# Kernel tuning notes

Measured on AMD Instinct MI355X. Metric: run time of the kernel, lower is better.

The kernel has to match this reference:

```python
import jax, jax.numpy as jnp
import numpy as np

B, E, XD = 2, 196608, 128     # batch, num edges (fine nodes), per-edge node feature dim
EIN, EOUT = 4, 128            # edge embedder dims
NREC = 12288                  # receiver (coarse) node count = 12*32^2
LIN, LOUT = EOUT + XD, 256    # output FFN dims


def setup_inputs() -> dict:
    key = jax.random.key(0)
    ks = jax.random.split(key, 8)
    w = lambda k, sh: jax.random.normal(k, sh, jnp.float32) * 0.05
    return {
        "x": jax.random.normal(ks[0], (B, E, XD), jnp.float32),
        "edge_attr": jax.random.normal(ks[1], (E, EIN), jnp.float32),
        "edge_index": jax.random.randint(ks[2], (2, E), 0, NREC, jnp.int32),
        # edge_embedder MLP: Linear(EIN,EOUT) -> SiLU -> Linear(EOUT,EOUT)
        "W1": w(ks[3], (EIN, EOUT)), "b1": jnp.zeros((EOUT,), jnp.float32),
        "W2": w(ks[4], (EOUT, EOUT)), "b2": jnp.zeros((EOUT,), jnp.float32),
        # output FeedForward: Linear(LIN,LOUT) -> SiLU -> Linear(LOUT,LOUT)
        "L1": w(ks[5], (LIN, LOUT)), "c1": jnp.zeros((LOUT,), jnp.float32),
        "L2": w(ks[6], (LOUT, LOUT)), "c2": jnp.zeros((LOUT,), jnp.float32),
    }


def reference(x, edge_attr, edge_index, W1, b1, W2, b2, L1, c1, L2, c2):
    # Edge MLP embed: [E, EIN] -> [E, EOUT]
    h = jax.nn.silu(edge_attr @ W1 + b1) @ W2 + b2
    # Broadcast edge features over batch and concat with per-edge node features
    ef = jnp.broadcast_to(h[None], (x.shape[0], h.shape[0], h.shape[1]))
    v = jnp.concatenate([ef, x], axis=-1)                 # [B, E, EOUT+XD]
    recv = edge_index[1]                                  # [E] in [0, NREC)
    # scatter_sum over edges -> receiver nodes, per batch
    agg = jax.vmap(lambda vb: jax.ops.segment_sum(vb, recv, num_segments=NREC))(v)  # [B, NREC, LIN]
    # Output FFN
    return jax.nn.silu(agg @ L1 + c1) @ L2 + c2           # [B, NREC, LOUT]
```

## Files before the change

### kernel.cpp

```cpp
#include <hip/hip_runtime.h>
#include <hip/hip_bf16.h>
#include <cstdint>
#include <cstddef>

#define B_     2
#define E_     196608
#define XD_    128
#define NREC_  12288
#define EOUT_  128
#define LIN_   256
#define LOUT_  256
#define M_     (B_ * NREC_)

typedef __attribute__((ext_vector_type(8))) short short8;
typedef __attribute__((ext_vector_type(4))) float f32x4;

__device__ __forceinline__ unsigned short f2bf(float f) {
    union { float f; unsigned u; } v; v.f = f;
    unsigned r = v.u + 0x7FFFu + ((v.u >> 16) & 1u);
    return (unsigned short)(r >> 16);
}

__global__ __launch_bounds__(256) void convert_w(const float* __restrict__ L1,
                                                 const float* __restrict__ L2,
                                                 unsigned short* __restrict__ L1T,
                                                 unsigned short* __restrict__ L2T) {
    int idx = blockIdx.x * 256 + threadIdx.x;
    int k = idx >> 8, n = idx & 255;
    L1T[n * 256 + k] = f2bf(L1[idx]);
    L2T[n * 256 + k] = f2bf(L2[idx]);
}

__global__ __launch_bounds__(256) void count_kernel(const int* __restrict__ recv,
                                                    int* __restrict__ cnt) {
    int e = blockIdx.x * 256 + threadIdx.x;
    if (e < E_) atomicAdd(&cnt[recv[e]], 1);
}

__global__ __launch_bounds__(1024) void scan_kernel(const int* __restrict__ cnt,
                                                    int* __restrict__ rowStart,
                                                    int* __restrict__ cursor) {
    __shared__ int sums[1024];
    int tid = threadIdx.x;
    int base = tid * 12;
    int local[12];
    int s = 0;
    #pragma unroll
    for (int j = 0; j < 12; ++j) { local[j] = s; s += cnt[base + j]; }
    sums[tid] = s;
    __syncthreads();
    for (int off = 1; off < 1024; off <<= 1) {
        int v = sums[tid];
        int add = (tid >= off) ? sums[tid - off] : 0;
        __syncthreads();
        sums[tid] = v + add;
        __syncthreads();
    }
    int excl = (tid == 0) ? 0 : sums[tid - 1];
    #pragma unroll
    for (int j = 0; j < 12; ++j) {
        int v = excl + local[j];
        rowStart[base + j] = v;
        cursor[base + j] = v;
    }
    if (tid == 1023) rowStart[NREC_] = excl + s;
}

__global__ __launch_bounds__(256) void fill_kernel(const int* __restrict__ recv,
                                                   int* __restrict__ cursor,
                                                   int* __restrict__ edge_ids) {
    int e = blockIdx.x * 256 + threadIdx.x;
    if (e < E_) {
        int p = atomicAdd(&cursor[recv[e]], 1);
        edge_ids[p] = e;
    }
}

__global__ __launch_bounds__(128) void gather_kernel(
        const float* __restrict__ x, const float* __restrict__ ea,
        const float* __restrict__ W1, const float* __restrict__ b1,
        const float* __restrict__ W2, const float* __restrict__ b2,
        const int* __restrict__ rowStart, const int* __restrict__ edge_ids,
        unsigned short* __restrict__ agg_bf) {
    __shared__ float s1row[128];
    int r = blockIdx.x;
    int c = threadIdx.x;
    int k0 = rowStart[r], k1 = rowStart[r + 1];
    float w10 = W1[c], w11 = W1[128 + c], w12 = W1[256 + c], w13 = W1[384 + c];
    float bb1 = b1[c];
    float accS1 = 0.f, accX0 = 0.f, accX1 = 0.f;
    for (int k = k0; k < k1; ++k) {
        int e = edge_ids[k];
        float e0 = ea[e * 4 + 0], e1 = ea[e * 4 + 1];
        float e2 = ea[e * 4 + 2], e3 = ea[e * 4 + 3];
        float p = fmaf(e0, w10, fmaf(e1, w11, fmaf(e2, w12, fmaf(e3, w13, bb1))));
        float sv = p / (1.f + __expf(-p));
        accS1 += sv;
        accX0 += x[(size_t)e * 128 + c];
        accX1 += x[(size_t)E_ * 128 + (size_t)e * 128 + c];
    }
    s1row[c] = accS1;
    __syncthreads();
    float accH = (float)(k1 - k0) * b2[c];
    for (int j = 0; j < 128; ++j)
        accH = fmaf(s1row[j], W2[j * 128 + c], accH);
    unsigned short hb = f2bf(accH);
    agg_bf[(size_t)r * 256 + c] = hb;
    agg_bf[(size_t)(NREC_ + r) * 256 + c] = hb;
    agg_bf[(size_t)r * 256 + 128 + c] = f2bf(accX0);
    agg_bf[(size_t)(NREC_ + r) * 256 + 128 + c] = f2bf(accX1);
}

__global__ __launch_bounds__(256) void ffn_kernel(
        const unsigned short* __restrict__ agg,
        const unsigned short* __restrict__ L1T, const float* __restrict__ c1,
        const unsigned short* __restrict__ L2T, const float* __restrict__ c2,
        float* __restrict__ out) {
    __shared__ unsigned short T[64][264];
    int tid  = threadIdx.x;
    int wave = tid >> 6;
    int lane = tid & 63;
    int quad = lane >> 4;
    int l16  = lane & 15;
    int m0 = blockIdx.x * 64 + wave * 16;

    short8 afrag[8];
    const unsigned short* aptr = agg + (size_t)(m0 + l16) * 256 + quad * 8;
    #pragma unroll
    for (int ks = 0; ks < 8; ++ks)
        afrag[ks] = *(const short8*)(aptr + ks * 32);

    #pragma unroll 2
    for (int nt = 0; nt < 16; ++nt) {
        f32x4 acc = {0.f, 0.f, 0.f, 0.f};
        const unsigned short* bptr = L1T + (size_t)(nt * 16 + l16) * 256 + quad * 8;
        #pragma unroll
        for (int ks = 0; ks < 8; ++ks) {
            short8 bfrag = *(const short8*)(bptr + ks * 32);
            acc = __builtin_amdgcn_mfma_f32_16x16x32_bf16(afrag[ks], bfrag, acc, 0, 0, 0);
        }
        #pragma unroll
        for (int rr = 0; rr < 4; ++rr) {
            int row = quad * 4 + rr;
            int col = nt * 16 + l16;
            float v = acc[rr] + c1[col];
            v = v / (1.f + __expf(-v));
            T[wave * 16 + row][col] = f2bf(v);
        }
    }
    __syncthreads();

    short8 afrag2[8];
    #pragma unroll
    for (int ks = 0; ks < 8; ++ks)
        afrag2[ks] = *(const short8*)&T[wave * 16 + l16][ks * 32 + quad * 8];

    #pragma unroll 2
    for (int nt = 0; nt < 16; ++nt) {
        f32x4 acc = {0.f, 0.f, 0.f, 0.f};
        const unsigned short* bptr = L2T + (size_t)(nt * 16 + l16) * 256 + quad * 8;
        #pragma unroll
        for (int ks = 0; ks < 8; ++ks) {
            short8 bfrag = *(const short8*)(bptr + ks * 32);
            acc = __builtin_amdgcn_mfma_f32_16x16x32_bf16(afrag2[ks], bfrag, acc, 0, 0, 0);
        }
        #pragma unroll
        for (int rr = 0; rr < 4; ++rr) {
            int row = m0 + quad * 4 + rr;
            int col = nt * 16 + l16;
            out[(size_t)row * 256 + col] = acc[rr] + c2[col];
        }
    }
}

extern "C" void kernel_launch(void* const* d_in, const int* in_sizes, int n_in,
                              void* d_out, int out_size, void* d_ws, size_t ws_size,
                              hipStream_t stream) {
    const float* x          = (const float*)d_in[0];
    const float* edge_attr  = (const float*)d_in[1];
    const int*   edge_index = (const int*)d_in[2];
    const float* W1 = (const float*)d_in[3];
    const float* b1 = (const float*)d_in[4];
    const float* W2 = (const float*)d_in[5];
    const float* b2 = (const float*)d_in[6];
    const float* L1 = (const float*)d_in[7];
    const float* c1 = (const float*)d_in[8];
    const float* L2 = (const float*)d_in[9];
    const float* c2 = (const float*)d_in[10];
    float* out = (float*)d_out;

    int* cnt      = (int*)d_ws;
    int* rowStart = cnt + NREC_;
    int* cursor   = rowStart + NREC_ + 4;
    int* edge_ids = cursor + NREC_;
    unsigned short* agg_bf = (unsigned short*)(edge_ids + E_);
    unsigned short* L1T = agg_bf + (size_t)M_ * 256;
    unsigned short* L2T = L1T + 256 * 256;

    const int* recv = edge_index + E_;

    hipMemsetAsync(cnt, 0, NREC_ * sizeof(int), stream);
    convert_w<<<256, 256, 0, stream>>>(L1, L2, L1T, L2T);
    count_kernel<<<(E_ + 255) / 256, 256, 0, stream>>>(recv, cnt);
    scan_kernel<<<1, 1024, 0, stream>>>(cnt, rowStart, cursor);
    fill_kernel<<<(E_ + 255) / 256, 256, 0, stream>>>(recv, cursor, edge_ids);
    gather_kernel<<<NREC_, 128, 0, stream>>>(x, edge_attr, W1, b1, W2, b2,
                                             rowStart, edge_ids, agg_bf);
    ffn_kernel<<<M_ / 64, 256, 0, stream>>>(agg_bf, L1T, c1, L2T, c2, out);
}
```

Measured before the change: 436.7 us.

## Fold edge-MLP second layer into L1 weights and unroll gather loop

Precomputes W2·L1[:128] as the first half of the transposed L1 weight, and b2·L1[:128] as a per-column vector scaled by receiver degree, so the gather kernel only sums SiLU activations. This removes the per-row 128x128 matvec and the shared-memory barrier from the gather kernel. The gather loop is also unrolled 8-wide, uses scalar edge ids via readfirstlane, and loads edge_attr as float4 to expose more memory-level parallelism. The cost is a slightly larger precompute kernel, plus bf16 rounding of the summed SiLU values before the folded weight is applied, which changes numerics a little.

```diff
diff --git a/kernel.cpp b/kernel.cpp
--- a/kernel.cpp
+++ b/kernel.cpp
@@ -21,14 +21,38 @@
     return (unsigned short)(r >> 16);
 }
 
-__global__ __launch_bounds__(256) void convert_w(const float* __restrict__ L1,
-                                                 const float* __restrict__ L2,
-                                                 unsigned short* __restrict__ L1T,
-                                                 unsigned short* __restrict__ L2T) {
-    int idx = blockIdx.x * 256 + threadIdx.x;
-    int k = idx >> 8, n = idx & 255;
-    L1T[n * 256 + k] = f2bf(L1[idx]);
-    L2T[n * 256 + k] = f2bf(L2[idx]);
+__global__ __launch_bounds__(256) void precompute(
+        const float* __restrict__ W2, const float* __restrict__ b2,
+        const float* __restrict__ L1, const float* __restrict__ L2,
+        unsigned short* __restrict__ L1T, unsigned short* __restrict__ L2T,
+        float* __restrict__ v) {
+    int bid = blockIdx.x;
+    int n = threadIdx.x;
+    if (bid < 128) {
+        int j = bid;
+        float a0 = 0.f, a1 = 0.f, a2 = 0.f, a3 = 0.f;
+        for (int c = 0; c < 128; c += 4) {
+            a0 = fmaf(W2[j * 128 + c + 0], L1[(c + 0) * 256 + n], a0);
+            a1 = fmaf(W2[j * 128 + c + 1], L1[(c + 1) * 256 + n], a1);
+            a2 = fmaf(W2[j * 128 + c + 2], L1[(c + 2) * 256 + n], a2);
+            a3 = fmaf(W2[j * 128 + c + 3], L1[(c + 3) * 256 + n], a3);
+        }
+        L1T[n * 256 + j] = f2bf((a0 + a1) + (a2 + a3));
+        if (j == 0) {
+            float s0 = 0.f, s1 = 0.f;
+            for (int c = 0; c < 128; c += 2) {
+                s0 = fmaf(b2[c + 0], L1[(c + 0) * 256 + n], s0);
+                s1 = fmaf(b2[c + 1], L1[(c + 1) * 256 + n], s1);
+            }
+            v[n] = s0 + s1;
+        }
+    } else if (bid < 256) {
+        int k = bid;
+        L1T[n * 256 + k] = f2bf(L1[k * 256 + n]);
+    } else {
+        int k = bid - 256;
+        L2T[n * 256 + k] = f2bf(L2[k * 256 + n]);
+    }
 }
 
 __global__ __launch_bounds__(256) void count_kernel(const int* __restrict__ recv,
@@ -50,18 +74,18 @@
     sums[tid] = s;
     __syncthreads();
     for (int off = 1; off < 1024; off <<= 1) {
-        int v = sums[tid];
+        int vv = sums[tid];
         int add = (tid >= off) ? sums[tid - off] : 0;
         __syncthreads();
-        sums[tid] = v + add;
+        sums[tid] = vv + add;
         __syncthreads();
     }
     int excl = (tid == 0) ? 0 : sums[tid - 1];
     #pragma unroll
     for (int j = 0; j < 12; ++j) {
-        int v = excl + local[j];
-        rowStart[base + j] = v;
-        cursor[base + j] = v;
+        int vv = excl + local[j];
+        rowStart[base + j] = vv;
+        cursor[base + j] = vv;
     }
     if (tid == 1023) rowStart[NREC_] = excl + s;
 }
@@ -79,42 +103,59 @@
 __global__ __launch_bounds__(128) void gather_kernel(
         const float* __restrict__ x, const float* __restrict__ ea,
         const float* __restrict__ W1, const float* __restrict__ b1,
-        const float* __restrict__ W2, const float* __restrict__ b2,
         const int* __restrict__ rowStart, const int* __restrict__ edge_ids,
         unsigned short* __restrict__ agg_bf) {
-    __shared__ float s1row[128];
     int r = blockIdx.x;
     int c = threadIdx.x;
-    int k0 = rowStart[r], k1 = rowStart[r + 1];
+    int k0 = __builtin_amdgcn_readfirstlane(rowStart[r]);
+    int k1 = __builtin_amdgcn_readfirstlane(rowStart[r + 1]);
     float w10 = W1[c], w11 = W1[128 + c], w12 = W1[256 + c], w13 = W1[384 + c];
     float bb1 = b1[c];
-    float accS1 = 0.f, accX0 = 0.f, accX1 = 0.f;
-    for (int k = k0; k < k1; ++k) {
-        int e = edge_ids[k];
-        float e0 = ea[e * 4 + 0], e1 = ea[e * 4 + 1];
-        float e2 = ea[e * 4 + 2], e3 = ea[e * 4 + 3];
-        float p = fmaf(e0, w10, fmaf(e1, w11, fmaf(e2, w12, fmaf(e3, w13, bb1))));
-        float sv = p / (1.f + __expf(-p));
-        accS1 += sv;
-        accX0 += x[(size_t)e * 128 + c];
-        accX1 += x[(size_t)E_ * 128 + (size_t)e * 128 + c];
-    }
-    s1row[c] = accS1;
-    __syncthreads();
-    float accH = (float)(k1 - k0) * b2[c];
-    for (int j = 0; j < 128; ++j)
-        accH = fmaf(s1row[j], W2[j * 128 + c], accH);
-    unsigned short hb = f2bf(accH);
-    agg_bf[(size_t)r * 256 + c] = hb;
-    agg_bf[(size_t)(NREC_ + r) * 256 + c] = hb;
-    agg_bf[(size_t)r * 256 + 128 + c] = f2bf(accX0);
-    agg_bf[(size_t)(NREC_ + r) * 256 + 128 + c] = f2bf(accX1);
+    const float* xb = x + (size_t)E_ * 128;
+    float accS = 0.f, aX0 = 0.f, aX1 = 0.f;
+    int k = k0;
+    for (; k + 8 <= k1; k += 8) {
+        int e[8];
+        #pragma unroll
+        for (int u = 0; u < 8; ++u)
+            e[u] = __builtin_amdgcn_readfirstlane(edge_ids[k + u]);
+        float xa[8], xc[8];
+        float4 q[8];
+        #pragma unroll
+        for (int u = 0; u < 8; ++u) {
+            xa[u] = x[(size_t)e[u] * 128 + c];
+            xc[u] = xb[(size_t)e[u] * 128 + c];
+            q[u] = *(const float4*)(ea + (size_t)e[u] * 4);
+        }
+        #pragma unroll
+        for (int u = 0; u < 8; ++u) {
+            float p = fmaf(q[u].x, w10, fmaf(q[u].y, w11,
+                      fmaf(q[u].z, w12, fmaf(q[u].w, w13, bb1))));
+            accS += p / (1.f + __expf(-p));
+            aX0 += xa[u];
+            aX1 += xc[u];
+        }
+    }
+    for (; k < k1; ++k) {
+        int e0 = __builtin_amdgcn_readfirstlane(edge_ids[k]);
+        float4 q = *(const float4*)(ea + (size_t)e0 * 4);
+        float p = fmaf(q.x, w10, fmaf(q.y, w11, fmaf(q.z, w12, fmaf(q.w, w13, bb1))));
+        accS += p / (1.f + __expf(-p));
+        aX0 += x[(size_t)e0 * 128 + c];
+        aX1 += xb[(size_t)e0 * 128 + c];
+    }
+    unsigned short sb = f2bf(accS);
+    agg_bf[(size_t)r * 256 + c] = sb;
+    agg_bf[(size_t)(NREC_ + r) * 256 + c] = sb;
+    agg_bf[(size_t)r * 256 + 128 + c] = f2bf(aX0);
+    agg_bf[(size_t)(NREC_ + r) * 256 + 128 + c] = f2bf(aX1);
 }
 
 __global__ __launch_bounds__(256) void ffn_kernel(
         const unsigned short* __restrict__ agg,
         const unsigned short* __restrict__ L1T, const float* __restrict__ c1,
         const unsigned short* __restrict__ L2T, const float* __restrict__ c2,
+        const float* __restrict__ v, const int* __restrict__ cnt,
         float* __restrict__ out) {
     __shared__ unsigned short T[64][264];
     int tid  = threadIdx.x;
@@ -124,6 +165,14 @@
     int l16  = lane & 15;
     int m0 = blockIdx.x * 64 + wave * 16;
 
+    float cntv[4];
+    #pragma unroll
+    for (int rr = 0; rr < 4; ++rr) {
+        int m = m0 + quad * 4 + rr;
+        int r = (m >= NREC_) ? m - NREC_ : m;
+        cntv[rr] = (float)cnt[r];
+    }
+
     short8 afrag[8];
     const unsigned short* aptr = agg + (size_t)(m0 + l16) * 256 + quad * 8;
     #pragma unroll
@@ -143,9 +192,9 @@
         for (int rr = 0; rr < 4; ++rr) {
             int row = quad * 4 + rr;
             int col = nt * 16 + l16;
-            float v = acc[rr] + c1[col];
-            v = v / (1.f + __expf(-v));
-            T[wave * 16 + row][col] = f2bf(v);
+            float pv = acc[rr] + c1[col] + cntv[rr] * v[col];
+            pv = pv / (1.f + __expf(-pv));
+            T[wave * 16 + row][col] = f2bf(pv);
         }
     }
     __syncthreads();
@@ -196,15 +245,16 @@
     unsigned short* agg_bf = (unsigned short*)(edge_ids + E_);
     unsigned short* L1T = agg_bf + (size_t)M_ * 256;
     unsigned short* L2T = L1T + 256 * 256;
+    float* v = (float*)(L2T + 256 * 256);
 
     const int* recv = edge_index + E_;
 
     hipMemsetAsync(cnt, 0, NREC_ * sizeof(int), stream);
-    convert_w<<<256, 256, 0, stream>>>(L1, L2, L1T, L2T);
+    precompute<<<512, 256, 0, stream>>>(W2, b2, L1, L2, L1T, L2T, v);
     count_kernel<<<(E_ + 255) / 256, 256, 0, stream>>>(recv, cnt);
     scan_kernel<<<1, 1024, 0, stream>>>(cnt, rowStart, cursor);
     fill_kernel<<<(E_ + 255) / 256, 256, 0, stream>>>(recv, cursor, edge_ids);
-    gather_kernel<<<NREC_, 128, 0, stream>>>(x, edge_attr, W1, b1, W2, b2,
+    gather_kernel<<<NREC_, 128, 0, stream>>>(x, edge_attr, W1, b1,
                                              rowStart, edge_ids, agg_bf);
-    ffn_kernel<<<M_ / 64, 256, 0, stream>>>(agg_bf, L1T, c1, L2T, c2, out);
-}
+    ffn_kernel<<<M_ / 64, 256, 0, stream>>>(agg_bf, L1T, c1, L2T, c2, v, cnt, out);
+}
```

Result: faster. 412.0 us (-5.7%).
